# Kernel tuning notes

Measured on AMD Instinct MI355X. Metric: run time of the kernel, lower is better.

Reference implementation:

```python
import jax, jax.numpy as jnp
import numpy as np

D_MODEL = 3072
N_HEADS = 24
MAX_LEN = 2048
ROPE_THETA = 10000.0
DH = D_MODEL // N_HEADS                  # 128
Q_PROJ = D_MODEL // 2                    # 1536
KV_PROJ = 2 * D_MODEL // 3               # 2048
NOPE = DH // 2                           # 64
ROPE = DH // 2                           # 64
EPS = 1e-5


def layernorm(x, w, b):
    m = jnp.mean(x, axis=-1, keepdims=True)
    v = jnp.mean(jnp.square(x - m), axis=-1, keepdims=True)
    return (x - m) / jnp.sqrt(v + EPS) * w + b


def rotate_half(x):
    h = x.shape[-1] // 2
    return jnp.concatenate([-x[..., h:], x[..., :h]], axis=-1)


def rope_tables(S):
    freqs = 1.0 / ROPE_THETA ** (jnp.arange(0, DH, 2, dtype=jnp.float32) / DH)  # [DH/2]
    emb = jnp.arange(S, dtype=jnp.float32)[:, None] * freqs[None, :]            # [S, DH/2]
    # torch: take first ROPE//2 freqs then .repeat(...,2) => tile along last axis
    cos = jnp.tile(jnp.cos(emb)[:, : ROPE // 2], (1, 2))  # [S, ROPE]
    sin = jnp.tile(jnp.sin(emb)[:, : ROPE // 2], (1, 2))
    return cos[None, None], sin[None, None]               # [1,1,S,ROPE]


def setup_inputs() -> dict:
    key = jax.random.key(0)
    ks = jax.random.split(key, 7)
    x = jax.random.normal(ks[0], (2, 2048, D_MODEL), dtype=jnp.float32)
    p = lambda k, shp: 0.01 * jax.random.normal(k, shp, dtype=jnp.float32)
    return {
        "x": x,
        "W_dq": p(ks[1], (D_MODEL, Q_PROJ)),
        "W_uq": p(ks[2], (Q_PROJ, D_MODEL)),
        "q_ln_w": jnp.ones((Q_PROJ,), jnp.float32),
        "q_ln_b": jnp.zeros((Q_PROJ,), jnp.float32),
        "W_dkv": p(ks[3], (D_MODEL, KV_PROJ + ROPE)),
        "W_ukv": p(ks[4], (KV_PROJ, D_MODEL + N_HEADS * NOPE)),
        "kv_ln_w": jnp.ones((KV_PROJ,), jnp.float32),
        "kv_ln_b": jnp.zeros((KV_PROJ,), jnp.float32),
        "W_o": p(ks[5], (D_MODEL, D_MODEL)),
    }


def reference(x, W_dq, W_uq, q_ln_w, q_ln_b, W_dkv, W_ukv, kv_ln_w, kv_ln_b, W_o):
    B, S, D = x.shape
    cos, sin = rope_tables(S)  # past_length=0, S_full=S

    # Q path: low-rank down/up projection
    cq = layernorm(x @ W_dq, q_ln_w, q_ln_b)          # [B,S,Q_PROJ]
    Q = (cq @ W_uq).reshape(B, S, N_HEADS, DH).transpose(0, 2, 1, 3)  # [B,H,S,DH]
    Q_nope, Q_rope = Q[..., :NOPE], Q[..., NOPE:]
    Q_rope = Q_rope * cos + rotate_half(Q_rope) * sin

    # KV path
    compressed_kv = x @ W_dkv                          # [B,S,KV_PROJ+ROPE]
    KV_lora = layernorm(compressed_kv[..., :KV_PROJ], kv_ln_w, kv_ln_b)
    K_rope = compressed_kv[..., KV_PROJ:]              # [B,S,ROPE]
    KV = (KV_lora @ W_ukv).reshape(B, S, N_HEADS, DH + NOPE).transpose(0, 2, 1, 3)
    K_nope, V = KV[..., :NOPE], KV[..., NOPE:]         # [B,H,S,NOPE], [B,H,S,DH]

    K_rope = K_rope[:, None]                           # [B,1,S,ROPE] shared head
    K_rope = K_rope * cos + rotate_half(K_rope) * sin

    q = jnp.concatenate([Q_nope, Q_rope], axis=-1)     # [B,H,S,DH]
    # k = cat(K_nope, K_rope broadcast over heads)
    k = jnp.concatenate([K_nope, jnp.broadcast_to(K_rope, (B, N_HEADS, S, ROPE))], axis=-1)

    scale = 1.0 / jnp.sqrt(jnp.float32(DH))
    scores = jnp.einsum("bhqd,bhkd->bhqk", q, k) * scale
    causal = jnp.tril(jnp.ones((S, S), dtype=bool))
    scores = jnp.where(causal[None, None], scores, jnp.float32(-jnp.inf))
    attn = jax.nn.softmax(scores, axis=-1)
    out = jnp.einsum("bhqk,bhkd->bhqd", attn, V)
    out = out.transpose(0, 2, 1, 3).reshape(B, S, D)
    out = out @ W_o.T
    return out, compressed_kv
```

## Files before the change

### kernel.cpp

```cpp
#include <hip/hip_runtime.h>

typedef unsigned short u16;
typedef __attribute__((ext_vector_type(8))) short short8;
typedef __attribute__((ext_vector_type(4))) float f32x4;

#define NROWS   4096
#define S_LEN   2048
#define NHEADS  24
#define DMODEL  3072
#define QPROJ   1536
#define KVPROJ  2048
#define CKV_W   2112
#define UKV_N   4608

__device__ __forceinline__ float bf2f(u16 v) {
    unsigned u = ((unsigned)v) << 16; float f; __builtin_memcpy(&f, &u, 4); return f;
}
__device__ __forceinline__ u16 f2bf(float f) {
    unsigned u; __builtin_memcpy(&u, &f, 4);
    u = (u + 0x7FFFu + ((u >> 16) & 1u)) >> 16; return (u16)u;
}
__device__ __forceinline__ void async16(const u16* g, u16* l) {
    __builtin_amdgcn_global_load_lds((const __attribute__((address_space(1))) unsigned int*)g,
                                     (__attribute__((address_space(3))) unsigned int*)l,
                                     16, 0, 0);
}

__global__ void conv_bf16(const float* __restrict__ X, u16* __restrict__ Y, int n) {
    int i = (blockIdx.x * 256 + threadIdx.x) * 4;
    if (i >= n) return;
    float4 v = *(const float4*)(X + i);
    Y[i+0] = f2bf(v.x); Y[i+1] = f2bf(v.y); Y[i+2] = f2bf(v.z); Y[i+3] = f2bf(v.w);
}

__global__ void transpose_bf16(const float* __restrict__ W, u16* __restrict__ WT,
                               int K, int N, float scale) {
    __shared__ float t[32][33];
    int nb = blockIdx.x * 32, kb = blockIdx.y * 32;
    int c = threadIdx.x & 31, rq = threadIdx.x >> 5;
#pragma unroll
    for (int i = 0; i < 4; ++i) {
        int r = rq * 4 + i;
        t[r][c] = W[(size_t)(kb + r) * N + nb + c];
    }
    __syncthreads();
#pragma unroll
    for (int i = 0; i < 4; ++i) {
        int r = rq * 4 + i;
        WT[(size_t)(nb + r) * K + kb + c] = f2bf(t[c][r] * scale);
    }
}

__global__ __launch_bounds__(256) void ln_kernel(const float* __restrict__ X, int ldx,
                                                 const float* __restrict__ g,
                                                 const float* __restrict__ b,
                                                 u16* __restrict__ Y, int W) {
    int row = blockIdx.x;
    const float* x = X + (size_t)row * ldx;
    float s = 0.f, s2 = 0.f;
    for (int i = threadIdx.x; i < W; i += 256) { float v = x[i]; s += v; s2 += v * v; }
#pragma unroll
    for (int off = 32; off >= 1; off >>= 1) { s += __shfl_xor(s, off); s2 += __shfl_xor(s2, off); }
    __shared__ float red[8];
    int w = threadIdx.x >> 6;
    if ((threadIdx.x & 63) == 0) { red[w] = s; red[4 + w] = s2; }
    __syncthreads();
    s  = red[0] + red[1] + red[2] + red[3];
    s2 = red[4] + red[5] + red[6] + red[7];
    float mean = s / W;
    float var  = s2 / W - mean * mean;
    float rstd = rsqrtf(var + 1e-5f);
    u16* y = Y + (size_t)row * W;
    for (int i = threadIdx.x; i < W; i += 256)
        y[i] = f2bf((x[i] - mean) * rstd * g[i] + b[i]);
}

__global__ void rope_q_kernel(u16* __restrict__ Q) {
    int idx = blockIdx.x * 256 + threadIdx.x;
    int j = idx & 31; int t = idx >> 5; int h = t % NHEADS; int row = t / NHEADS;
    int s = row & (S_LEN - 1);
    float freq = __expf(-(float)j * (9.210340371976184f / 64.f));
    float ang = (float)s * freq;
    float c = cosf(ang), si = sinf(ang);
    u16* p = Q + (size_t)row * DMODEL + h * 128 + 64;
    float x1 = bf2f(p[j]), x2 = bf2f(p[j + 32]);
    p[j]      = f2bf(x1 * c - x2 * si);
    p[j + 32] = f2bf(x2 * c + x1 * si);
}

__global__ void rope_k_kernel(const float* __restrict__ ckv, u16* __restrict__ kr) {
    int idx = blockIdx.x * 256 + threadIdx.x;
    int j = idx & 31; int row = idx >> 5;
    int s = row & (S_LEN - 1);
    float freq = __expf(-(float)j * (9.210340371976184f / 64.f));
    float ang = (float)s * freq;
    float c = cosf(ang), si = sinf(ang);
    const float* src = ckv + (size_t)row * CKV_W + KVPROJ;
    float x1 = src[j], x2 = src[j + 32];
    kr[(size_t)row * 64 + j]      = f2bf(x1 * c - x2 * si);
    kr[(size_t)row * 64 + j + 32] = f2bf(x2 * c + x1 * si);
}

__global__ __launch_bounds__(256) void pack_k(const u16* __restrict__ KVb,
                                              const u16* __restrict__ kr,
                                              u16* __restrict__ Kp) {
    int bh = blockIdx.y, bb = bh / NHEADS, h = bh % NHEADS;
    int s0 = blockIdx.x * 64;
    int t = threadIdx.x;
    size_t base = (size_t)bb * S_LEN;
#pragma unroll
    for (int it = 0; it < 4; ++it) {
        int j = it * 256 + t;
        int r = j >> 4, cb = (j & 15) * 8;
        int s = s0 + r;
        uint4 v;
        if (cb < 64) v = *(const uint4*)&KVb[(base + s) * UKV_N + h * 192 + cb];
        else         v = *(const uint4*)&kr[(base + s) * 64 + (cb - 64)];
        *(uint4*)&Kp[((size_t)bh * S_LEN + s) * 128 + cb] = v;
    }
}

__global__ __launch_bounds__(256) void pack_v(const u16* __restrict__ KVb,
                                              u16* __restrict__ Vt) {
    __shared__ u16 tile[64][136];
    int bh = blockIdx.y, bb = bh / NHEADS, h = bh % NHEADS;
    int s0 = blockIdx.x * 64;
    int t = threadIdx.x;
    size_t base = (size_t)bb * S_LEN;
#pragma unroll
    for (int it = 0; it < 4; ++it) {
        int j = it * 256 + t;
        int r = j >> 4, cb = (j & 15) * 8;
        *(uint4*)&tile[r][cb] = *(const uint4*)&KVb[(base + s0 + r) * UKV_N + h * 192 + 64 + cb];
    }
    __syncthreads();
#pragma unroll
    for (int it = 0; it < 4; ++it) {
        int j = it * 256 + t;
        int d = j >> 3, sb = (j & 7) * 8;
        u16 tmp[8];
#pragma unroll
        for (int e = 0; e < 8; ++e) tmp[e] = tile[sb + e][d];
        *(uint4*)&Vt[((size_t)bh * 128 + d) * S_LEN + s0 + sb] = *(uint4*)tmp;
    }
}

template<bool OUT_BF16>
__global__ __launch_bounds__(256) void gemm_nt(const u16* __restrict__ A,
                                               const u16* __restrict__ B,
                                               void* __restrict__ Cv,
                                               int M, int N, int K) {
    __shared__ u16 a_lds[2][128][32];
    __shared__ u16 b_lds[2][128][32];
    int m0 = blockIdx.y * 128, n0 = blockIdx.x * 128;
    int tid = threadIdx.x, lane = tid & 63, w = tid >> 6;
    int wm = w >> 1, wn = w & 1;
    int srow = lane >> 2;
    int kx = (lane >> 4) & 2;
    int scol = ((lane & 3) ^ kx) * 8;
    int r0 = w * 32 + srow, r1 = w * 32 + 16 + srow;
    const u16* A0 = A + (size_t)(m0 + r0) * K + scol;
    const u16* A1 = A + (size_t)(m0 + r1) * K + scol;
    int bn0 = n0 + r0; if (bn0 >= N) bn0 = N - 1;
    int bn1 = n0 + r1; if (bn1 >= N) bn1 = N - 1;
    const u16* B0 = B + (size_t)bn0 * K + scol;
    const u16* B1 = B + (size_t)bn1 * K + scol;
    char* aB = (char*)&a_lds[0][0][0];
    char* bB = (char*)&b_lds[0][0][0];
    int d0 = w * 2048, d1 = w * 2048 + 1024;
    int cb = ((lane >> 4) * 16) ^ ((lane & 8) << 2);

    f32x4 acc[4][4] = {};
    async16(A0, (u16*)(aB + d0)); async16(A1, (u16*)(aB + d1));
    async16(B0, (u16*)(bB + d0)); async16(B1, (u16*)(bB + d1));
    __syncthreads();
    int buf = 0;
    for (int kb = 0; kb < K; kb += 32) {
        if (kb + 32 < K) {
            int ob = (buf ^ 1) * 8192;
            async16(A0 + kb + 32, (u16*)(aB + ob + d0));
            async16(A1 + kb + 32, (u16*)(aB + ob + d1));
            async16(B0 + kb + 32, (u16*)(bB + ob + d0));
            async16(B1 + kb + 32, (u16*)(bB + ob + d1));
        }
        const char* ab = aB + buf * 8192;
        const char* bb = bB + buf * 8192;
        short8 af[4], bf[4];
#pragma unroll
        for (int i = 0; i < 4; ++i) {
            af[i] = *(const short8*)(ab + (wm * 64 + i * 16 + (lane & 15)) * 64 + cb);
            bf[i] = *(const short8*)(bb + (wn * 64 + i * 16 + (lane & 15)) * 64 + cb);
        }
#pragma unroll
        for (int i = 0; i < 4; ++i)
#pragma unroll
            for (int j = 0; j < 4; ++j)
                acc[i][j] = __builtin_amdgcn_mfma_f32_16x16x32_bf16(af[i], bf[j], acc[i][j], 0, 0, 0);
        __syncthreads();
        buf ^= 1;
    }
#pragma unroll
    for (int i = 0; i < 4; ++i) {
        int row = m0 + wm * 64 + i * 16 + ((lane >> 4) << 2);
#pragma unroll
        for (int j = 0; j < 4; ++j) {
            int col = n0 + wn * 64 + j * 16 + (lane & 15);
            if (col < N) {
#pragma unroll
                for (int r = 0; r < 4; ++r) {
                    if (OUT_BF16) ((u16*)Cv)[(size_t)(row + r) * N + col] = f2bf(acc[i][j][r]);
                    else          ((float*)Cv)[(size_t)(row + r) * N + col] = acc[i][j][r];
                }
            }
        }
    }
}

__global__ __launch_bounds__(256) void attn_kernel(const u16* __restrict__ Qb,
                                                   const u16* __restrict__ Kp,
                                                   const u16* __restrict__ Vt,
                                                   u16* __restrict__ AO) {
    __shared__ u16 k_lds[2][64][128];
    __shared__ u16 v_lds[2][128][64];
    __shared__ u16 p_lds[4][16][72];
    int qx = (int)gridDim.x - 1 - (int)blockIdx.x;
    int q0 = qx * 64;
    int bh = blockIdx.y; int bb = bh / NHEADS, h = bh % NHEADS;
    int tid = threadIdx.x, lane = tid & 63, w = tid >> 6;
    size_t base = (size_t)bb * S_LEN;
    size_t bhS = (size_t)bh * S_LEN;

    short8 qf[4];
    {
        int qrow = q0 + w * 16 + (lane & 15);
        const u16* qp = Qb + (base + qrow) * DMODEL + h * 128 + ((lane >> 4) * 8);
#pragma unroll
        for (int ks = 0; ks < 4; ++ks) qf[ks] = *(const short8*)(qp + ks * 32);
    }

    const char* Kbyte = (const char*)Kp;
    const char* Vbyte = (const char*)Vt;
    char* kB = (char*)&k_lds[0][0][0];
    char* vB = (char*)&v_lds[0][0][0];
    size_t ksrc[4], vsrc[4];
    int kd[4];
#pragma unroll
    for (int is = 0; is < 4; ++is) {
        int j = is * 256 + tid;
        int r = j >> 4;
        int cbs = ((j & 15) * 16) ^ ((r & 7) << 4);
        ksrc[is] = (bhS + r) * 256 + cbs;
        int d = j >> 3;
        int kbs = (((j & 7) ^ (d & 7)) * 16);
        vsrc[is] = ((size_t)bh * 128 + d) * (S_LEN * 2) + kbs;
        kd[is] = (is * 256 + w * 64) * 16;
    }

    f32x4 acc_o[8] = {};
    float m_run[4], l_run[4];
#pragma unroll
    for (int r = 0; r < 4; ++r) { m_run[r] = -1e30f; l_run[r] = 0.f; }

    int ntiles = qx + 1;
#pragma unroll
    for (int is = 0; is < 4; ++is) async16((const u16*)(Kbyte + ksrc[is]), (u16*)(kB + kd[is]));
#pragma unroll
    for (int is = 0; is < 4; ++is) async16((const u16*)(Vbyte + vsrc[is]), (u16*)(vB + kd[is]));
    __syncthreads();
    int buf = 0;

    for (int t = 0; t < ntiles; ++t) {
        if (t + 1 < ntiles) {
            size_t kv1 = (size_t)(t + 1) * 64;
            int ob = (buf ^ 1) * 16384;
#pragma unroll
            for (int is = 0; is < 4; ++is)
                async16((const u16*)(Kbyte + ksrc[is] + kv1 * 256), (u16*)(kB + ob + kd[is]));
#pragma unroll
            for (int is = 0; is < 4; ++is)
                async16((const u16*)(Vbyte + vsrc[is] + kv1 * 2), (u16*)(vB + ob + kd[is]));
        }
        const char* kcur = kB + buf * 16384;
        const char* vcur = vB + buf * 16384;

        f32x4 sc[4];
        __builtin_amdgcn_s_setprio(1);
#pragma unroll
        for (int nb = 0; nb < 4; ++nb) {
            f32x4 a = {};
            int row = nb * 16 + (lane & 15);
            const char* kb_ = kcur + row * 256;
            int x = (row & 7) << 4;
#pragma unroll
            for (int ks = 0; ks < 4; ++ks) {
                short8 kf = *(const short8*)(kb_ + ((ks * 64 + (lane >> 4) * 16) ^ x));
                a = __builtin_amdgcn_mfma_f32_16x16x32_bf16(qf[ks], kf, a, 0, 0, 0);
            }
            sc[nb] = a;
        }
        __builtin_amdgcn_s_setprio(0);

        if (t == qx) {
            int kv0 = t * 64;
            int qg = q0 + w * 16 + ((lane >> 4) << 2);
#pragma unroll
            for (int nb = 0; nb < 4; ++nb) {
                int kc = kv0 + nb * 16 + (lane & 15);
#pragma unroll
                for (int r = 0; r < 4; ++r)
                    if (kc > qg + r) sc[nb][r] = -1e30f;
            }
        }
        float rmax[4];
#pragma unroll
        for (int r = 0; r < 4; ++r)
            rmax[r] = fmaxf(fmaxf(sc[0][r], sc[1][r]), fmaxf(sc[2][r], sc[3][r]));
#pragma unroll
        for (int off = 1; off < 16; off <<= 1)
#pragma unroll
            for (int r = 0; r < 4; ++r) rmax[r] = fmaxf(rmax[r], __shfl_xor(rmax[r], off));

        float mnew[4], fac[4], rsum[4];
#pragma unroll
        for (int r = 0; r < 4; ++r) {
            mnew[r] = fmaxf(m_run[r], rmax[r]);
            fac[r] = __expf(m_run[r] - mnew[r]);
            rsum[r] = 0.f;
        }
#pragma unroll
        for (int nb = 0; nb < 4; ++nb)
#pragma unroll
            for (int r = 0; r < 4; ++r) {
                float p = __expf(sc[nb][r] - mnew[r]);
                sc[nb][r] = p; rsum[r] += p;
            }
#pragma unroll
        for (int off = 1; off < 16; off <<= 1)
#pragma unroll
            for (int r = 0; r < 4; ++r) rsum[r] += __shfl_xor(rsum[r], off);
#pragma unroll
        for (int r = 0; r < 4; ++r) {
            l_run[r] = l_run[r] * fac[r] + rsum[r];
            m_run[r] = mnew[r];
        }
#pragma unroll
        for (int db = 0; db < 8; ++db)
#pragma unroll
            for (int r = 0; r < 4; ++r) acc_o[db][r] *= fac[r];

#pragma unroll
        for (int nb = 0; nb < 4; ++nb)
#pragma unroll
            for (int r = 0; r < 4; ++r)
                p_lds[w][((lane >> 4) << 2) + r][nb * 16 + (lane & 15)] = f2bf(sc[nb][r]);
        __builtin_amdgcn_sched_barrier(0);
        __builtin_amdgcn_s_setprio(1);
#pragma unroll
        for (int ks = 0; ks < 2; ++ks) {
            short8 pf = *(const short8*)&p_lds[w][lane & 15][ks * 32 + (lane >> 4) * 8];
#pragma unroll
            for (int db = 0; db < 8; ++db) {
                int row = db * 16 + (lane & 15);
                const char* vb_ = vcur + row * 128;
                short8 vf = *(const short8*)(vb_ + ((ks * 64 + (lane >> 4) * 16) ^ ((row & 7) << 4)));
                acc_o[db] = __builtin_amdgcn_mfma_f32_16x16x32_bf16(pf, vf, acc_o[db], 0, 0, 0);
            }
        }
        __builtin_amdgcn_s_setprio(0);
        __syncthreads();
        buf ^= 1;
    }

    int orow = q0 + w * 16 + ((lane >> 4) << 2);
#pragma unroll
    for (int db = 0; db < 8; ++db)
#pragma unroll
        for (int r = 0; r < 4; ++r) {
            float o = acc_o[db][r] / l_run[r];
            AO[(base + orow + r) * DMODEL + h * 128 + db * 16 + (lane & 15)] = f2bf(o);
        }
}

extern "C" void kernel_launch(void* const* d_in, const int* in_sizes, int n_in,
                              void* d_out, int out_size, void* d_ws, size_t ws_size,
                              hipStream_t stream) {
    (void)in_sizes; (void)n_in; (void)out_size; (void)ws_size;
    const float* x      = (const float*)d_in[0];
    const float* W_dq   = (const float*)d_in[1];
    const float* W_uq   = (const float*)d_in[2];
    const float* q_ln_w = (const float*)d_in[3];
    const float* q_ln_b = (const float*)d_in[4];
    const float* W_dkv  = (const float*)d_in[5];
    const float* W_ukv  = (const float*)d_in[6];
    const float* kv_ln_w= (const float*)d_in[7];
    const float* kv_ln_b= (const float*)d_in[8];
    const float* W_o    = (const float*)d_in[9];

    float* out = (float*)d_out;
    float* ckv = out + (size_t)NROWS * DMODEL;

    char* ws = (char*)d_ws;
    const size_t OFF_WDQT  = 0;
    const size_t OFF_WUQT  = 9437184;
    const size_t OFF_WDKVT = 18874368;
    const size_t OFF_WUKVT = 31850496;
    const size_t OFF_WO    = 50724864;
    const size_t OFF_XB    = 69599232;
    const size_t OFF_QB    = 94765056;
    const size_t OFF_KVB   = 119930880;
    const size_t OFF_KR    = 157679616;
    const size_t OFF_SLABA = 158203904;
    const size_t OFF_SLABB = 183369728;
    const size_t OFF_KP    = 0;
    const size_t OFF_VT    = OFF_XB;

    u16* Wdq_t  = (u16*)(ws + OFF_WDQT);
    u16* Wuq_t  = (u16*)(ws + OFF_WUQT);
    u16* Wdkv_t = (u16*)(ws + OFF_WDKVT);
    u16* Wukv_t = (u16*)(ws + OFF_WUKVT);
    u16* Wo_b   = (u16*)(ws + OFF_WO);
    u16* xb     = (u16*)(ws + OFF_XB);
    u16* qb     = (u16*)(ws + OFF_QB);
    u16* KVb    = (u16*)(ws + OFF_KVB);
    u16* kr     = (u16*)(ws + OFF_KR);
    float* t0   = (float*)(ws + OFF_SLABA);
    u16* ao     = (u16*)(ws + OFF_SLABA);
    u16* cq     = (u16*)(ws + OFF_SLABB);
    u16* kvl    = (u16*)(ws + OFF_SLABB);
    u16* Kp     = (u16*)(ws + OFF_KP);
    u16* Vt     = (u16*)(ws + OFF_VT);

    const float SCALE = 0.08838834764831845f;

    transpose_bf16<<<dim3(QPROJ / 32, DMODEL / 32), 256, 0, stream>>>(W_dq,  Wdq_t,  DMODEL, QPROJ, 1.0f);
    transpose_bf16<<<dim3(DMODEL / 32, QPROJ / 32), 256, 0, stream>>>(W_uq,  Wuq_t,  QPROJ, DMODEL, SCALE);
    transpose_bf16<<<dim3(CKV_W / 32, DMODEL / 32), 256, 0, stream>>>(W_dkv, Wdkv_t, DMODEL, CKV_W, 1.0f);
    transpose_bf16<<<dim3(UKV_N / 32, KVPROJ / 32), 256, 0, stream>>>(W_ukv, Wukv_t, KVPROJ, UKV_N, 1.0f);
    conv_bf16<<<9216, 256, 0, stream>>>(W_o, Wo_b, DMODEL * DMODEL);
    conv_bf16<<<12288, 256, 0, stream>>>(x, xb, NROWS * DMODEL);

    gemm_nt<false><<<dim3(QPROJ / 128, NROWS / 128), 256, 0, stream>>>(xb, Wdq_t, t0, NROWS, QPROJ, DMODEL);
    ln_kernel<<<NROWS, 256, 0, stream>>>(t0, QPROJ, q_ln_w, q_ln_b, cq, QPROJ);
    gemm_nt<true><<<dim3(DMODEL / 128, NROWS / 128), 256, 0, stream>>>(cq, Wuq_t, qb, NROWS, DMODEL, QPROJ);
    rope_q_kernel<<<12288, 256, 0, stream>>>(qb);

    gemm_nt<false><<<dim3((CKV_W + 127) / 128, NROWS / 128), 256, 0, stream>>>(xb, Wdkv_t, ckv, NROWS, CKV_W, DMODEL);
    ln_kernel<<<NROWS, 256, 0, stream>>>(ckv, CKV_W, kv_ln_w, kv_ln_b, kvl, KVPROJ);
    rope_k_kernel<<<512, 256, 0, stream>>>(ckv, kr);
    gemm_nt<true><<<dim3(UKV_N / 128, NROWS / 128), 256, 0, stream>>>(kvl, Wukv_t, KVb, NROWS, UKV_N, KVPROJ);

    pack_k<<<dim3(S_LEN / 64, 2 * NHEADS), 256, 0, stream>>>(KVb, kr, Kp);
    pack_v<<<dim3(S_LEN / 64, 2 * NHEADS), 256, 0, stream>>>(KVb, Vt);

    attn_kernel<<<dim3(S_LEN / 64, 2 * NHEADS), 256, 0, stream>>>(qb, Kp, Vt, ao);

    gemm_nt<false><<<dim3(DMODEL / 128, NROWS / 128), 256, 0, stream>>>(ao, Wo_b, out, NROWS, DMODEL, DMODEL);
}
```

Before: 742.0 us.

## Use 128-row query blocks with 8 waves sharing single-buffered KV tiles

Each attention block now covers 128 query rows with 512 threads (8 waves), so every K/V tile loaded into LDS is reused by twice as many query rows. This halves the global K/V traffic per query. The double-buffered prefetch is removed: each tile is loaded and then synchronised before use, which exposes load latency. Waves whose causal range ends earlier skip the extra tile but still wait at the barriers.

```diff
diff --git a/kernel.cpp b/kernel.cpp
--- a/kernel.cpp
+++ b/kernel.cpp
@@ -216,15 +216,15 @@
     }
 }
 
-__global__ __launch_bounds__(256) void attn_kernel(const u16* __restrict__ Qb,
+__global__ __launch_bounds__(512) void attn_kernel(const u16* __restrict__ Qb,
                                                    const u16* __restrict__ Kp,
                                                    const u16* __restrict__ Vt,
                                                    u16* __restrict__ AO) {
-    __shared__ u16 k_lds[2][64][128];
-    __shared__ u16 v_lds[2][128][64];
-    __shared__ u16 p_lds[4][16][72];
-    int qx = (int)gridDim.x - 1 - (int)blockIdx.x;
-    int q0 = qx * 64;
+    __shared__ u16 k_lds[64][128];
+    __shared__ u16 v_lds[128][64];
+    __shared__ u16 p_lds[8][16][72];
+    int qxb = (int)gridDim.x - 1 - (int)blockIdx.x;
+    int q0 = qxb * 128;
     int bh = blockIdx.y; int bb = bh / NHEADS, h = bh % NHEADS;
     int tid = threadIdx.x, lane = tid & 63, w = tid >> 6;
     size_t base = (size_t)bb * S_LEN;
@@ -240,20 +240,20 @@
 
     const char* Kbyte = (const char*)Kp;
     const char* Vbyte = (const char*)Vt;
-    char* kB = (char*)&k_lds[0][0][0];
-    char* vB = (char*)&v_lds[0][0][0];
-    size_t ksrc[4], vsrc[4];
-    int kd[4];
-#pragma unroll
-    for (int is = 0; is < 4; ++is) {
-        int j = is * 256 + tid;
+    char* kB = (char*)&k_lds[0][0];
+    char* vB = (char*)&v_lds[0][0];
+    size_t ksrc[2], vsrc[2];
+    int kd[2];
+#pragma unroll
+    for (int is = 0; is < 2; ++is) {
+        int j = is * 512 + tid;
         int r = j >> 4;
         int cbs = ((j & 15) * 16) ^ ((r & 7) << 4);
         ksrc[is] = (bhS + r) * 256 + cbs;
         int d = j >> 3;
         int kbs = (((j & 7) ^ (d & 7)) * 16);
         vsrc[is] = ((size_t)bh * 128 + d) * (S_LEN * 2) + kbs;
-        kd[is] = (is * 256 + w * 64) * 16;
+        kd[is] = (is * 512 + w * 64) * 16;
     }
 
     f32x4 acc_o[8] = {};
@@ -261,114 +261,106 @@
 #pragma unroll
     for (int r = 0; r < 4; ++r) { m_run[r] = -1e30f; l_run[r] = 0.f; }
 
-    int ntiles = qx + 1;
-#pragma unroll
-    for (int is = 0; is < 4; ++is) async16((const u16*)(Kbyte + ksrc[is]), (u16*)(kB + kd[is]));
-#pragma unroll
-    for (int is = 0; is < 4; ++is) async16((const u16*)(Vbyte + vsrc[is]), (u16*)(vB + kd[is]));
-    __syncthreads();
-    int buf = 0;
+    int ntiles = 2 * qxb + 2;
+    int wave_nt = ((q0 + w * 16 + 15) >> 6) + 1;
 
     for (int t = 0; t < ntiles; ++t) {
-        if (t + 1 < ntiles) {
-            size_t kv1 = (size_t)(t + 1) * 64;
-            int ob = (buf ^ 1) * 16384;
-#pragma unroll
-            for (int is = 0; is < 4; ++is)
-                async16((const u16*)(Kbyte + ksrc[is] + kv1 * 256), (u16*)(kB + ob + kd[is]));
-#pragma unroll
-            for (int is = 0; is < 4; ++is)
-                async16((const u16*)(Vbyte + vsrc[is] + kv1 * 2), (u16*)(vB + ob + kd[is]));
+        size_t kv0 = (size_t)t * 64;
+#pragma unroll
+        for (int is = 0; is < 2; ++is)
+            async16((const u16*)(Kbyte + ksrc[is] + kv0 * 256), (u16*)(kB + kd[is]));
+#pragma unroll
+        for (int is = 0; is < 2; ++is)
+            async16((const u16*)(Vbyte + vsrc[is] + kv0 * 2), (u16*)(vB + kd[is]));
+        __syncthreads();
+
+        if (t < wave_nt) {
+            f32x4 sc[4];
+            __builtin_amdgcn_s_setprio(1);
+#pragma unroll
+            for (int nb = 0; nb < 4; ++nb) {
+                f32x4 a = {};
+                int row = nb * 16 + (lane & 15);
+                const char* kb_ = kB + row * 256;
+                int x = (row & 7) << 4;
+#pragma unroll
+                for (int ks = 0; ks < 4; ++ks) {
+                    short8 kf = *(const short8*)(kb_ + ((ks * 64 + (lane >> 4) * 16) ^ x));
+                    a = __builtin_amdgcn_mfma_f32_16x16x32_bf16(qf[ks], kf, a, 0, 0, 0);
+                }
+                sc[nb] = a;
+            }
+            __builtin_amdgcn_s_setprio(0);
+
+            if (t + 1 == wave_nt) {
+                int kvb = t * 64;
+                int qg = q0 + w * 16 + ((lane >> 4) << 2);
+#pragma unroll
+                for (int nb = 0; nb < 4; ++nb) {
+                    int kc = kvb + nb * 16 + (lane & 15);
+#pragma unroll
+                    for (int r = 0; r < 4; ++r)
+                        if (kc > qg + r) sc[nb][r] = -1e30f;
+                }
+            }
+            float rmax[4];
+#pragma unroll
+            for (int r = 0; r < 4; ++r)
+                rmax[r] = fmaxf(fmaxf(sc[0][r], sc[1][r]), fmaxf(sc[2][r], sc[3][r]));
+#pragma unroll
+            for (int off = 1; off < 16; off <<= 1)
+#pragma unroll
+                for (int r = 0; r < 4; ++r) rmax[r] = fmaxf(rmax[r], __shfl_xor(rmax[r], off));
+
+            float mnew[4], fac[4], rsum[4];
+#pragma unroll
+            for (int r = 0; r < 4; ++r) {
+                mnew[r] = fmaxf(m_run[r], rmax[r]);
+                fac[r] = __expf(m_run[r] - mnew[r]);
+                rsum[r] = 0.f;
+            }
+#pragma unroll
+            for (int nb = 0; nb < 4; ++nb)
+#pragma unroll
+                for (int r = 0; r < 4; ++r) {
+                    float p = __expf(sc[nb][r] - mnew[r]);
+                    sc[nb][r] = p; rsum[r] += p;
+                }
+#pragma unroll
+            for (int off = 1; off < 16; off <<= 1)
+#pragma unroll
+                for (int r = 0; r < 4; ++r) rsum[r] += __shfl_xor(rsum[r], off);
+#pragma unroll
+            for (int r = 0; r < 4; ++r) {
+                l_run[r] = l_run[r] * fac[r] + rsum[r];
+                m_run[r] = mnew[r];
+            }
+#pragma unroll
+            for (int db = 0; db < 8; ++db)
+#pragma unroll
+                for (int r = 0; r < 4; ++r) acc_o[db][r] *= fac[r];
+
+#pragma unroll
+            for (int nb = 0; nb < 4; ++nb)
+#pragma unroll
+                for (int r = 0; r < 4; ++r)
+                    p_lds[w][((lane >> 4) << 2) + r][nb * 16 + (lane & 15)] = f2bf(sc[nb][r]);
+            __builtin_amdgcn_sched_barrier(0);
+            __builtin_amdgcn_s_setprio(1);
+#pragma unroll
+            for (int ks = 0; ks < 2; ++ks) {
+                short8 pf = *(const short8*)&p_lds[w][lane & 15][ks * 32 + (lane >> 4) * 8];
+#pragma unroll
+                for (int db = 0; db < 8; ++db) {
+                    int row = db * 16 + (lane & 15);
+                    const char* vb_ = vB + row * 128;
+                    short8 vf = *(const short8*)(vb_ + ((ks * 64 + (lane >> 4) * 16) ^ ((row & 7) << 4)));
+                    acc_o[db] = __builtin_amdgcn_mfma_f32_16x16x32_bf16(pf, vf, acc_o[db], 0, 0, 0);
+                }
+            }
+            __builtin_amdgcn_s_setprio(0);
         }
-        const char* kcur = kB + buf * 16384;
-        const char* vcur = vB + buf * 16384;
-
-        f32x4 sc[4];
-        __builtin_amdgcn_s_setprio(1);
-#pragma unroll
-        for (int nb = 0; nb < 4; ++nb) {
-            f32x4 a = {};
-            int row = nb * 16 + (lane & 15);
-            const char* kb_ = kcur + row * 256;
-            int x = (row & 7) << 4;
-#pragma unroll
-            for (int ks = 0; ks < 4; ++ks) {
-                short8 kf = *(const short8*)(kb_ + ((ks * 64 + (lane >> 4) * 16) ^ x));
-                a = __builtin_amdgcn_mfma_f32_16x16x32_bf16(qf[ks], kf, a, 0, 0, 0);
-            }
-            sc[nb] = a;
-        }
-        __builtin_amdgcn_s_setprio(0);
-
-        if (t == qx) {
-            int kv0 = t * 64;
-            int qg = q0 + w * 16 + ((lane >> 4) << 2);
-#pragma unroll
-            for (int nb = 0; nb < 4; ++nb) {
-                int kc = kv0 + nb * 16 + (lane & 15);
-#pragma unroll
-                for (int r = 0; r < 4; ++r)
-                    if (kc > qg + r) sc[nb][r] = -1e30f;
-            }
-        }
-        float rmax[4];
-#pragma unroll
-        for (int r = 0; r < 4; ++r)
-            rmax[r] = fmaxf(fmaxf(sc[0][r], sc[1][r]), fmaxf(sc[2][r], sc[3][r]));
-#pragma unroll
-        for (int off = 1; off < 16; off <<= 1)
-#pragma unroll
-            for (int r = 0; r < 4; ++r) rmax[r] = fmaxf(rmax[r], __shfl_xor(rmax[r], off));
-
-        float mnew[4], fac[4], rsum[4];
-#pragma unroll
-        for (int r = 0; r < 4; ++r) {
-            mnew[r] = fmaxf(m_run[r], rmax[r]);
-            fac[r] = __expf(m_run[r] - mnew[r]);
-            rsum[r] = 0.f;
-        }
-#pragma unroll
-        for (int nb = 0; nb < 4; ++nb)
-#pragma unroll
-            for (int r = 0; r < 4; ++r) {
-                float p = __expf(sc[nb][r] - mnew[r]);
-                sc[nb][r] = p; rsum[r] += p;
-            }
-#pragma unroll
-        for (int off = 1; off < 16; off <<= 1)
-#pragma unroll
-            for (int r = 0; r < 4; ++r) rsum[r] += __shfl_xor(rsum[r], off);
-#pragma unroll
-        for (int r = 0; r < 4; ++r) {
-            l_run[r] = l_run[r] * fac[r] + rsum[r];
-            m_run[r] = mnew[r];
-        }
-#pragma unroll
-        for (int db = 0; db < 8; ++db)
-#pragma unroll
-            for (int r = 0; r < 4; ++r) acc_o[db][r] *= fac[r];
-
-#pragma unroll
-        for (int nb = 0; nb < 4; ++nb)
-#pragma unroll
-            for (int r = 0; r < 4; ++r)
-                p_lds[w][((lane >> 4) << 2) + r][nb * 16 + (lane & 15)] = f2bf(sc[nb][r]);
-        __builtin_amdgcn_sched_barrier(0);
-        __builtin_amdgcn_s_setprio(1);
-#pragma unroll
-        for (int ks = 0; ks < 2; ++ks) {
-            short8 pf = *(const short8*)&p_lds[w][lane & 15][ks * 32 + (lane >> 4) * 8];
-#pragma unroll
-            for (int db = 0; db < 8; ++db) {
-                int row = db * 16 + (lane & 15);
-                const char* vb_ = vcur + row * 128;
-                short8 vf = *(const short8*)(vb_ + ((ks * 64 + (lane >> 4) * 16) ^ ((row & 7) << 4)));
-                acc_o[db] = __builtin_amdgcn_mfma_f32_16x16x32_bf16(pf, vf, acc_o[db], 0, 0, 0);
-            }
-        }
-        __builtin_amdgcn_s_setprio(0);
         __syncthreads();
-        buf ^= 1;
     }
 
     int orow = q0 + w * 16 + ((lane >> 4) << 2);
@@ -452,7 +444,7 @@
     pack_k<<<dim3(S_LEN / 64, 2 * NHEADS), 256, 0, stream>>>(KVb, kr, Kp);
     pack_v<<<dim3(S_LEN / 64, 2 * NHEADS), 256, 0, stream>>>(KVb, Vt);
 
-    attn_kernel<<<dim3(S_LEN / 64, 2 * NHEADS), 256, 0, stream>>>(qb, Kp, Vt, ao);
+    attn_kernel<<<dim3(S_LEN / 128, 2 * NHEADS), 512, 0, stream>>>(qb, Kp, Vt, ao);
 
     gemm_nt<false><<<dim3(DMODEL / 128, NROWS / 128), 256, 0, stream>>>(ao, Wo_b, out, NROWS, DMODEL, DMODEL);
 }
```

Measured after the change: 702.3 us. 1.06x faster.
